# Performance work log

Hardware: AMD Instinct MI355X
Metric: run time of the kernel (lower is better)

The kernel has to match this reference:

```python
import jax, jax.numpy as jnp
import numpy as np

N, IN_DIM, LATENT = 2048, 32, 64
GUMBEL_SCALE = 0.3


def setup_inputs() -> dict:
    key = jax.random.key(0)
    ks = jax.random.split(key, 10)
    x = jax.random.normal(ks[0], (N, IN_DIM), dtype=jnp.float32)
    in_adj = (jax.random.uniform(ks[1], (N, N)) < 0.01).astype(jnp.float32)
    # symmetric Gumbel(0, 0.3) noise on off-diagonal (triu offset 1, mirrored)
    u = jax.random.uniform(ks[2], (N, N), minval=1e-6, maxval=1.0 - 1e-6)
    g = -GUMBEL_SCALE * jnp.log(-jnp.log(u))
    gu = jnp.triu(g, 1)
    gumbel_noise = gu + gu.T
    s = 1.0 / np.sqrt(IN_DIM)
    W_ne = jax.random.uniform(ks[3], (IN_DIM, LATENT), minval=-s, maxval=s)
    b_ne = jnp.zeros((LATENT,), jnp.float32)
    s2 = 1.0 / np.sqrt(2 * LATENT)
    W_e1a = jax.random.uniform(ks[4], (LATENT, LATENT), minval=-s2, maxval=s2)
    W_e1b = jax.random.uniform(ks[5], (LATENT, LATENT), minval=-s2, maxval=s2)
    b_e1 = jnp.zeros((LATENT,), jnp.float32)
    s3 = 1.0 / np.sqrt(LATENT)
    w_e2 = jax.random.uniform(ks[6], (LATENT,), minval=-s3, maxval=s3)
    b_e2 = jnp.zeros((), jnp.float32)
    return dict(x=x, in_adj=in_adj, gumbel_noise=gumbel_noise,
                W_ne=W_ne, b_ne=b_ne, W_e1a=W_e1a, W_e1b=W_e1b,
                b_e1=b_e1, w_e2=w_e2, b_e2=b_e2)


def reference(x, in_adj, gumbel_noise, W_ne, b_ne, W_e1a, W_e1b, b_e1, w_e2, b_e2):
    lrelu = lambda v: jax.nn.leaky_relu(v, 0.01)
    # node encoding for edges: Linear + LeakyReLU  [N, L]
    z = lrelu(x @ W_ne + b_ne)
    # edge_encode on concat(z_i, z_j): split first Linear's weight into two
    # halves so the [N, N, 2L] concat is never materialized.
    zi = z @ W_e1a  # [N, L] (source-node half)
    zj = z @ W_e1b  # [N, L] (target-node half)
    h = lrelu(zi[:, None, :] + zj[None, :, :] + b_e1)  # [N, N, L]
    logit = jnp.einsum('ijl,l->ij', h, w_e2) + b_e2    # [N, N]
    edge_p = jax.nn.sigmoid(logit)
    # perturb_edge_prob: log -> add symmetric gumbel -> exp
    pert_edge_p = jnp.exp(jnp.log(edge_p + 1e-8) + gumbel_noise)
    # debug_step == 1, hard=False: return soft perturbed edge probs [N, N]
    return pert_edge_p
```

## Files before the change

kernel.cpp:

```cpp
#include <hip/hip_runtime.h>

#define N 2048
#define IN_DIM 32
#define L 64
#define LDSS 68

__global__ __launch_bounds__(64) void precompute_kernel(
    const float* __restrict__ x,
    const float* __restrict__ W_ne,
    const float* __restrict__ b_ne,
    const float* __restrict__ W_e1a,
    const float* __restrict__ W_e1b,
    const float* __restrict__ b_e1,
    const float* __restrict__ w_e2,
    const float* __restrict__ b_e2,
    float* __restrict__ zi_g,
    float* __restrict__ zjb_g,
    float* __restrict__ A_g,
    float* __restrict__ B_g,
    float* __restrict__ w2p_g)
{
    const int i = blockIdx.x;
    const int l = threadIdx.x;
    __shared__ float zrow[L];

    float acc = b_ne[l];
    #pragma unroll
    for (int k = 0; k < IN_DIM; ++k)
        acc = fmaf(x[i * IN_DIM + k], W_ne[k * L + l], acc);
    float z = fmaxf(acc, 0.01f * acc);
    zrow[l] = z;
    __syncthreads();

    float vi = 0.0f, vj = b_e1[l];
    #pragma unroll 8
    for (int m = 0; m < L; ++m) {
        float zm = zrow[m];
        vi = fmaf(zm, W_e1a[m * L + l], vi);
        vj = fmaf(zm, W_e1b[m * L + l], vj);
    }
    zi_g[i * L + l]  = vi;
    zjb_g[i * L + l] = vj;

    float w = w_e2[l];
    float ta = w * vi, tb = w * vj;
    #pragma unroll
    for (int off = 32; off > 0; off >>= 1) {
        ta += __shfl_xor(ta, off);
        tb += __shfl_xor(tb, off);
    }
    if (l == 0) {
        A_g[i] = 0.505f * ta;
        B_g[i] = 0.505f * tb + b_e2[0];
    }
    if (i == 0) w2p_g[l] = 0.495f * w;
}

__global__ __launch_bounds__(256) void edge_kernel(
    const float* __restrict__ zi_g,
    const float* __restrict__ zjb_g,
    const float* __restrict__ A_g,
    const float* __restrict__ B_g,
    const float* __restrict__ w2p_g,
    const float* __restrict__ gumbel,
    float* __restrict__ out)
{
    __shared__ float zi_s[64 * LDSS];
    __shared__ float zj_s[64 * LDSS];

    const int jb = blockIdx.x * 64;
    const int ib = blockIdx.y * 64;
    const int t  = threadIdx.x;
    const int tx = t & 15;
    const int ty = t >> 4;

    #pragma unroll
    for (int rep = 0; rep < 4; ++rep) {
        int idx  = rep * 256 + t;
        int row  = idx >> 4;
        int col4 = (idx & 15) * 4;
        *(float4*)&zi_s[row * LDSS + col4] = *(const float4*)&zi_g[(ib + row) * L + col4];
        *(float4*)&zj_s[row * LDSS + col4] = *(const float4*)&zjb_g[(jb + row) * L + col4];
    }
    __syncthreads();

    float acc[4][4];
    #pragma unroll
    for (int a = 0; a < 4; ++a)
        #pragma unroll
        for (int b = 0; b < 4; ++b) acc[a][b] = 0.0f;

    const float4* __restrict__ w4 = (const float4*)w2p_g;

    #pragma unroll
    for (int lq = 0; lq < 16; ++lq) {
        float4 w = w4[lq];
        float4 ai[4], bj[4];
        #pragma unroll
        for (int r = 0; r < 4; ++r) {
            ai[r] = *(const float4*)&zi_s[(ty + 16 * r) * LDSS + lq * 4];
            bj[r] = *(const float4*)&zj_s[(tx + 16 * r) * LDSS + lq * 4];
        }
        #pragma unroll
        for (int ri = 0; ri < 4; ++ri)
            #pragma unroll
            for (int rj = 0; rj < 4; ++rj) {
                float sx = ai[ri].x + bj[rj].x;
                float sy = ai[ri].y + bj[rj].y;
                float sz = ai[ri].z + bj[rj].z;
                float sw = ai[ri].w + bj[rj].w;
                float a0 = acc[ri][rj];
                a0 = fmaf(w.x, fabsf(sx), a0);
                a0 = fmaf(w.y, fabsf(sy), a0);
                a0 = fmaf(w.z, fabsf(sz), a0);
                a0 = fmaf(w.w, fabsf(sw), a0);
                acc[ri][rj] = a0;
            }
    }

    float Ai[4], Bj[4];
    #pragma unroll
    for (int r = 0; r < 4; ++r) {
        Ai[r] = A_g[ib + ty + 16 * r];
        Bj[r] = B_g[jb + tx + 16 * r];
    }

    #pragma unroll
    for (int ri = 0; ri < 4; ++ri) {
        int gi = ib + ty + 16 * ri;
        #pragma unroll
        for (int rj = 0; rj < 4; ++rj) {
            int gj = jb + tx + 16 * rj;
            float logit = Ai[ri] + Bj[rj] + acc[ri][rj];
            float p = 1.0f / (1.0f + __expf(-logit));
            float g = gumbel[(size_t)gi * N + gj];
            out[(size_t)gi * N + gj] = (p + 1e-8f) * __expf(g);
        }
    }
}

extern "C" void kernel_launch(void* const* d_in, const int* in_sizes, int n_in,
                              void* d_out, int out_size, void* d_ws, size_t ws_size,
                              hipStream_t stream) {
    const float* x      = (const float*)d_in[0];
    const float* gumbel = (const float*)d_in[2];
    const float* W_ne   = (const float*)d_in[3];
    const float* b_ne   = (const float*)d_in[4];
    const float* W_e1a  = (const float*)d_in[5];
    const float* W_e1b  = (const float*)d_in[6];
    const float* b_e1   = (const float*)d_in[7];
    const float* w_e2   = (const float*)d_in[8];
    const float* b_e2   = (const float*)d_in[9];
    float* out = (float*)d_out;

    char* ws = (char*)d_ws;
    float* zi_g  = (float*)(ws);
    float* zjb_g = (float*)(ws + 512 * 1024);
    float* A_g   = (float*)(ws + 1024 * 1024);
    float* B_g   = (float*)(ws + 1024 * 1024 + 8 * 1024);
    float* w2p_g = (float*)(ws + 1024 * 1024 + 16 * 1024);

    precompute_kernel<<<N, 64, 0, stream>>>(x, W_ne, b_ne, W_e1a, W_e1b, b_e1,
                                            w_e2, b_e2, zi_g, zjb_g, A_g, B_g, w2p_g);
    edge_kernel<<<dim3(N / 64, N / 64), 256, 0, stream>>>(zi_g, zjb_g, A_g, B_g,
                                                          w2p_g, gumbel, out);
}
```

Before: 111.4 us.

## Use packed fp16 with fdot2 for the pairwise edge MLP inner loop

Stores the per-node zi/zj projections and scaled second-layer weights in fp16, then computes the pairwise sum, abs and weighted accumulation with packed half2 adds and the fdot2 instruction, accumulating in fp32. This halves LDS footprint and load traffic and roughly halves the VALU instruction count of the N*N*L inner loop, which dominates compute. The cost is reduced precision in the logits, which could exceed tolerance for larger activations.

```diff
diff --git a/kernel.cpp b/kernel.cpp
--- a/kernel.cpp
+++ b/kernel.cpp
@@ -3,7 +3,27 @@
 #define N 2048
 #define IN_DIM 32
 #define L 64
-#define LDSS 68
+#define LDSH 72
+
+typedef _Float16 half_t;
+typedef _Float16 h2 __attribute__((ext_vector_type(2)));
+typedef _Float16 h8 __attribute__((ext_vector_type(8)));
+union H8 { h8 v; h2 h[4]; };
+
+__device__ inline h2 habs2(h2 a) {
+    unsigned u; __builtin_memcpy(&u, &a, 4);
+    u &= 0x7FFF7FFFu;
+    __builtin_memcpy(&a, &u, 4);
+    return a;
+}
+
+__device__ inline float dot2acc(h2 a, h2 b, float c) {
+#if __has_builtin(__builtin_amdgcn_fdot2)
+    return __builtin_amdgcn_fdot2(a, b, c, false);
+#else
+    return c + (float)a.x * (float)b.x + (float)a.y * (float)b.y;
+#endif
+}
 
 __global__ __launch_bounds__(64) void precompute_kernel(
     const float* __restrict__ x,
@@ -14,11 +34,11 @@
     const float* __restrict__ b_e1,
     const float* __restrict__ w_e2,
     const float* __restrict__ b_e2,
-    float* __restrict__ zi_g,
-    float* __restrict__ zjb_g,
+    half_t* __restrict__ zi_h,
+    half_t* __restrict__ zjb_h,
     float* __restrict__ A_g,
     float* __restrict__ B_g,
-    float* __restrict__ w2p_g)
+    half_t* __restrict__ w2p_h)
 {
     const int i = blockIdx.x;
     const int l = threadIdx.x;
@@ -39,8 +59,8 @@
         vi = fmaf(zm, W_e1a[m * L + l], vi);
         vj = fmaf(zm, W_e1b[m * L + l], vj);
     }
-    zi_g[i * L + l]  = vi;
-    zjb_g[i * L + l] = vj;
+    zi_h[i * L + l]  = (half_t)vi;
+    zjb_h[i * L + l] = (half_t)vj;
 
     float w = w_e2[l];
     float ta = w * vi, tb = w * vj;
@@ -53,20 +73,20 @@
         A_g[i] = 0.505f * ta;
         B_g[i] = 0.505f * tb + b_e2[0];
     }
-    if (i == 0) w2p_g[l] = 0.495f * w;
+    if (i == 0) w2p_h[l] = (half_t)(0.495f * w);
 }
 
 __global__ __launch_bounds__(256) void edge_kernel(
-    const float* __restrict__ zi_g,
-    const float* __restrict__ zjb_g,
+    const half_t* __restrict__ zi_h,
+    const half_t* __restrict__ zjb_h,
     const float* __restrict__ A_g,
     const float* __restrict__ B_g,
-    const float* __restrict__ w2p_g,
+    const half_t* __restrict__ w2p_h,
     const float* __restrict__ gumbel,
     float* __restrict__ out)
 {
-    __shared__ float zi_s[64 * LDSS];
-    __shared__ float zj_s[64 * LDSS];
+    __shared__ half_t zi_s[64 * LDSH];
+    __shared__ half_t zj_s[64 * LDSH];
 
     const int jb = blockIdx.x * 64;
     const int ib = blockIdx.y * 64;
@@ -75,12 +95,12 @@
     const int ty = t >> 4;
 
     #pragma unroll
-    for (int rep = 0; rep < 4; ++rep) {
-        int idx  = rep * 256 + t;
-        int row  = idx >> 4;
-        int col4 = (idx & 15) * 4;
-        *(float4*)&zi_s[row * LDSS + col4] = *(const float4*)&zi_g[(ib + row) * L + col4];
-        *(float4*)&zj_s[row * LDSS + col4] = *(const float4*)&zjb_g[(jb + row) * L + col4];
+    for (int rep = 0; rep < 2; ++rep) {
+        int idx = rep * 256 + t;
+        int row = idx >> 3;
+        int c   = idx & 7;
+        *(float4*)&zi_s[row * LDSH + c * 8] = *(const float4*)&zi_h[(ib + row) * L + c * 8];
+        *(float4*)&zj_s[row * LDSH + c * 8] = *(const float4*)&zjb_h[(jb + row) * L + c * 8];
     }
     __syncthreads();
 
@@ -90,30 +110,26 @@
         #pragma unroll
         for (int b = 0; b < 4; ++b) acc[a][b] = 0.0f;
 
-    const float4* __restrict__ w4 = (const float4*)w2p_g;
-
     #pragma unroll
-    for (int lq = 0; lq < 16; ++lq) {
-        float4 w = w4[lq];
-        float4 ai[4], bj[4];
+    for (int lq = 0; lq < 8; ++lq) {
+        H8 w;
+        w.v = *(const h8*)&w2p_h[lq * 8];
+        H8 ai[4], bj[4];
         #pragma unroll
         for (int r = 0; r < 4; ++r) {
-            ai[r] = *(const float4*)&zi_s[(ty + 16 * r) * LDSS + lq * 4];
-            bj[r] = *(const float4*)&zj_s[(tx + 16 * r) * LDSS + lq * 4];
+            ai[r].v = *(const h8*)&zi_s[(ty + 16 * r) * LDSH + lq * 8];
+            bj[r].v = *(const h8*)&zj_s[(tx + 16 * r) * LDSH + lq * 8];
         }
         #pragma unroll
         for (int ri = 0; ri < 4; ++ri)
             #pragma unroll
             for (int rj = 0; rj < 4; ++rj) {
-                float sx = ai[ri].x + bj[rj].x;
-                float sy = ai[ri].y + bj[rj].y;
-                float sz = ai[ri].z + bj[rj].z;
-                float sw = ai[ri].w + bj[rj].w;
                 float a0 = acc[ri][rj];
-                a0 = fmaf(w.x, fabsf(sx), a0);
-                a0 = fmaf(w.y, fabsf(sy), a0);
-                a0 = fmaf(w.z, fabsf(sz), a0);
-                a0 = fmaf(w.w, fabsf(sw), a0);
+                #pragma unroll
+                for (int c = 0; c < 4; ++c) {
+                    h2 s = ai[ri].h[c] + bj[rj].h[c];
+                    a0 = dot2acc(habs2(s), w.h[c], a0);
+                }
                 acc[ri][rj] = a0;
             }
     }
@@ -154,14 +170,14 @@
     float* out = (float*)d_out;
 
     char* ws = (char*)d_ws;
-    float* zi_g  = (float*)(ws);
-    float* zjb_g = (float*)(ws + 512 * 1024);
-    float* A_g   = (float*)(ws + 1024 * 1024);
-    float* B_g   = (float*)(ws + 1024 * 1024 + 8 * 1024);
-    float* w2p_g = (float*)(ws + 1024 * 1024 + 16 * 1024);
+    half_t* zi_h  = (half_t*)(ws);
+    half_t* zjb_h = (half_t*)(ws + 256 * 1024);
+    float*  A_g   = (float*)(ws + 512 * 1024);
+    float*  B_g   = (float*)(ws + 512 * 1024 + 8 * 1024);
+    half_t* w2p_h = (half_t*)(ws + 512 * 1024 + 16 * 1024);
 
     precompute_kernel<<<N, 64, 0, stream>>>(x, W_ne, b_ne, W_e1a, W_e1b, b_e1,
-                                            w_e2, b_e2, zi_g, zjb_g, A_g, B_g, w2p_g);
-    edge_kernel<<<dim3(N / 64, N / 64), 256, 0, stream>>>(zi_g, zjb_g, A_g, B_g,
-                                                          w2p_g, gumbel, out);
+                                            w_e2, b_e2, zi_h, zjb_h, A_g, B_g, w2p_h);
+    edge_kernel<<<dim3(N / 64, N / 64), 256, 0, stream>>>(zi_h, zjb_h, A_g, B_g,
+                                                          w2p_h, gumbel, out);
 }
```

Result: no change. 113.0 us (+1.4%).
